# Optimization experiments

Measured on AMD Instinct MI355X. Metric: run time of the kernel, lower is better.

Reference implementation:

```python
import jax, jax.numpy as jnp
import numpy as np


def setup_inputs() -> dict:
    key = jax.random.key(0)
    ks = jax.random.split(key, 5)
    B, S, D, H, DK = 2, 2048, 1024, 16, 64
    scale = 1.0 / np.sqrt(D)
    return {
        "x": jax.random.normal(ks[0], (B, S, D), dtype=jnp.float32),
        "Wq": jax.random.normal(ks[1], (H, D, DK), dtype=jnp.float32) * scale,
        "Wk": jax.random.normal(ks[2], (H, D, DK), dtype=jnp.float32) * scale,
        "Wv": jax.random.normal(ks[3], (H, D, DK), dtype=jnp.float32) * scale,
        "Wo": jax.random.normal(ks[4], (D, D), dtype=jnp.float32) * scale,
    }


def reference(x, Wq, Wk, Wv, Wo):
    # x: (B, S, D); Wq/Wk/Wv: (H, D, d_k); Wo: (D, D) torch-Linear convention (y = c @ Wo.T)
    B, S, D = x.shape
    H, _, dk = Wq.shape
    Q = jnp.einsum('bsd,hdk->bhsk', x, Wq)  # (B,H,S,dk)
    K = jnp.einsum('bsd,hdk->bhsk', x, Wk)
    V = jnp.einsum('bsd,hdk->bhsk', x, Wv)
    scores = jnp.einsum('bhqk,bhsk->bhqs', Q, K) / jnp.sqrt(jnp.float32(dk))  # (B,H,S,S)
    causal = jnp.tril(jnp.ones((S, S), dtype=bool))
    scores = jnp.where(causal[None, None, :, :], scores, -jnp.inf)
    weights = jax.nn.softmax(scores, axis=-1)
    out = jnp.einsum('bhqs,bhsk->bhqk', weights, V)  # (B,H,S,dk)
    concat = out.transpose(0, 2, 1, 3).reshape(B, S, H * dk)  # heads concatenated h-major
    return concat @ Wo.T
```

## Files before the change

### kernel.cpp

```cpp
#include <hip/hip_runtime.h>

typedef unsigned short u16;
typedef unsigned int u32;
typedef __bf16 bf16x8 __attribute__((ext_vector_type(8)));
typedef float f32x4 __attribute__((ext_vector_type(4)));
typedef u16 u16x8 __attribute__((ext_vector_type(8)));
typedef u16 u16x4 __attribute__((ext_vector_type(4)));
typedef u32 u32x4 __attribute__((ext_vector_type(4)));

#define NH 16
#define DKK 64
#define SQ 2048
#define DD 1024

#define AS1 __attribute__((address_space(1)))
#define AS3 __attribute__((address_space(3)))

#define QSCALE 0.1803368925f
#define CBIAS 8.0f

#define WAIT4 do { asm volatile("s_waitcnt vmcnt(4)" ::: "memory"); \
                   __builtin_amdgcn_sched_barrier(0); } while (0)
#define WAIT0 do { asm volatile("s_waitcnt vmcnt(0)" ::: "memory"); \
                   __builtin_amdgcn_sched_barrier(0); } while (0)
#define BAR   __builtin_amdgcn_s_barrier()

__device__ inline u16 f2bf(float f) {
  union { float f; u32 u; } v; v.f = f;
  u32 u = v.u;
  u += 0x7FFFu + ((u >> 16) & 1u);
  return (u16)(u >> 16);
}

__device__ __forceinline__ u32 cvtpk(float lo, float hi) {
  u32 r;
  asm("v_cvt_pk_bf16_f32 %0, %1, %2" : "=v"(r) : "v"(lo), "v"(hi));
  return r;
}

__device__ inline u16x8 cvt8(const float* p) {
  float4 a = *(const float4*)p;
  float4 b = *(const float4*)(p + 4);
  u16x8 v;
  v[0] = f2bf(a.x); v[1] = f2bf(a.y); v[2] = f2bf(a.z); v[3] = f2bf(a.w);
  v[4] = f2bf(b.x); v[5] = f2bf(b.y); v[6] = f2bf(b.z); v[7] = f2bf(b.w);
  return v;
}

__device__ __forceinline__ void gload16(const u16* g, u16* l) {
  __builtin_amdgcn_global_load_lds((const AS1 u32*)(const void*)g,
                                   (AS3 u32*)(void*)l, 16, 0, 0);
}

__global__ __launch_bounds__(256) void prep_kernel(const float* __restrict__ x,
                                                   u16* __restrict__ xb,
                                                   const float* __restrict__ Wo,
                                                   u16* __restrict__ Wob,
                                                   const float* __restrict__ Wq,
                                                   const float* __restrict__ Wk,
                                                   const float* __restrict__ Wv,
                                                   u16* __restrict__ WT) {
  __shared__ u16 sm[64][72];
  int bid = blockIdx.x;
  int tid = threadIdx.x;
  if (bid < 2560) {
    const float* src; u16* dst; size_t base;
    if (bid < 2048) { src = x;  dst = xb;  base = (size_t)bid * 2048; }
    else            { src = Wo; dst = Wob; base = (size_t)(bid - 2048) * 2048; }
    size_t off = base + (size_t)tid * 8;
    *(u16x8*)&dst[off] = cvt8(&src[off]);
    return;
  }
  int wid = bid - 2560;
  int t = wid >> 8;
  int rem = wid & 255;
  int h = rem >> 4;
  int d0 = (rem & 15) * 64;
  const float* src = (t == 0) ? Wq : (t == 1) ? Wk : Wv;
  for (int j = 0; j < 2; ++j) {
    int idx = tid + j * 256;
    int r = idx >> 3;
    int c0 = (idx & 7) * 8;
    *(u16x8*)&sm[r][c0] = cvt8(&src[(h * DD + d0 + r) * DKK + c0]);
  }
  __syncthreads();
  for (int j = 0; j < 2; ++j) {
    int idx = tid + j * 256;
    int r2 = idx >> 3;
    int c0 = (idx & 7) * 8;
    u16x8 vv;
    for (int i = 0; i < 8; ++i) vv[i] = sm[c0 + i][r2];
    int n = t * 1024 + h * 64 + r2;
    *(u16x8*)&WT[n * DD + d0 + c0] = vv;
  }
}

__global__ __launch_bounds__(256) void gemm128(const u16* __restrict__ A,
                                               const u16* __restrict__ Bm,
                                               int mode,
                                               u16* __restrict__ o0,
                                               u16* __restrict__ o1,
                                               u16* __restrict__ o2,
                                               float* __restrict__ of) {
  __shared__ u16 As[2][128 * 32];
  __shared__ u16 Bs[2][128 * 32];
  const int K = 1024;
  int m0 = blockIdx.x * 128;
  int n0 = blockIdx.y * 128;
  int tid = threadIdx.x;
  int w = tid >> 6, l = tid & 63;
  int lg = l >> 4, lr = l & 15;
  int wr = w >> 1, wc = w & 1;

  int srow = w * 32 + (l >> 2);
  int sg = (l & 3) ^ ((l >> 3) & 3);
  const u16* gA = A + (size_t)(m0 + srow) * K + sg * 8;
  const u16* gB = Bm + (size_t)(n0 + srow) * K + sg * 8;
  int gsw = (lr >> 1) & 3;

  #define GSTAGE(buf, k0)                              \
    do {                                               \
      gload16(gA + (k0), &As[buf][w * 1024]);          \
      gload16(gA + (k0) + 16 * K, &As[buf][w * 1024 + 512]); \
      gload16(gB + (k0), &Bs[buf][w * 1024]);          \
      gload16(gB + (k0) + 16 * K, &Bs[buf][w * 1024 + 512]); \
    } while (0)

  f32x4 acc[4][4] = {};
  GSTAGE(0, 0);
  for (int kt = 0; kt < 32; ++kt) {
    int buf = kt & 1;
    if (kt < 31) { GSTAGE(buf ^ 1, (kt + 1) * 32); WAIT4; }
    else         { WAIT0; }
    BAR;
    bf16x8 a[4], b[4];
    #pragma unroll
    for (int m = 0; m < 4; ++m)
      a[m] = *(const bf16x8*)&As[buf][(wr * 64 + m * 16 + lr) * 32 + ((lg ^ gsw) * 8)];
    #pragma unroll
    for (int n = 0; n < 4; ++n)
      b[n] = *(const bf16x8*)&Bs[buf][(wc * 64 + n * 16 + lr) * 32 + ((lg ^ gsw) * 8)];
    #pragma unroll
    for (int m = 0; m < 4; ++m)
      #pragma unroll
      for (int n = 0; n < 4; ++n)
        acc[m][n] = __builtin_amdgcn_mfma_f32_16x16x32_bf16(a[m], b[n], acc[m][n], 0, 0, 0);
    BAR;
  }
  #undef GSTAGE

  if (mode == 1) {
    int mbase = m0 + wr * 64 + lg * 4;
    int nbase = n0 + wc * 64 + lr;
    #pragma unroll
    for (int m = 0; m < 4; ++m)
      #pragma unroll
      for (int n = 0; n < 4; ++n)
        #pragma unroll
        for (int rr = 0; rr < 4; ++rr)
          of[(size_t)(mbase + m * 16 + rr) * 1024 + nbase + n * 16] = acc[m][n][rr];
  } else {
    int t = n0 >> 10;
    int h = (((n0 & 1023) + wc * 64) >> 6);
    int bq = m0 >> 11;
    int sbase = (m0 & 2047) + wr * 64 + lg * 4;
    if (t < 2) {
      float sc = (t == 0) ? QSCALE : 1.0f;
      u16* o = (t == 0) ? o0 : o1;
      u16* op = o + (size_t)(bq * NH + h) * SQ * DKK;
      #pragma unroll
      for (int m = 0; m < 4; ++m)
        #pragma unroll
        for (int n = 0; n < 4; ++n)
          #pragma unroll
          for (int rr = 0; rr < 4; ++rr)
            op[(size_t)(sbase + m * 16 + rr) * DKK + n * 16 + lr] = f2bf(acc[m][n][rr] * sc);
    } else {
      u16* op = o2 + (size_t)(bq * NH + h) * DKK * SQ;
      int Sb = (m0 & 2047) + wr * 64;
      #pragma unroll
      for (int m = 0; m < 4; ++m)
        #pragma unroll
        for (int n = 0; n < 4; ++n) {
          u16x4 vv;
          #pragma unroll
          for (int rr = 0; rr < 4; ++rr) vv[rr] = f2bf(acc[m][n][rr]);
          *(u16x4*)&op[(size_t)(n * 16 + lr) * SQ + Sb + (m >> 1) * 32 + lg * 8 + (m & 1) * 4] = vv;
        }
    }
  }
}

__global__ __launch_bounds__(256) void attn_kernel(const u16* __restrict__ Q,
                                                   const u16* __restrict__ Kg,
                                                   const u16* __restrict__ Vt,
                                                   u16* __restrict__ Cc) {
  __shared__ u16 Ks[2][64 * 64];
  __shared__ u16 Vs[2][64 * 64];
  int bh = blockIdx.x;
  int y = blockIdx.y;
  int a = y & 7, bsel = y >> 3;
  int s = (bsel == 0) ? 2 * a : (bsel == 1) ? 2 * a + 1
        : (bsel == 2) ? 30 - 2 * a : 31 - 2 * a;
  int tid = threadIdx.x;
  int w = tid >> 6, l = tid & 63;
  int lg = l >> 4, lr = l & 15;
  const u16* Qp = Q + (size_t)bh * SQ * DKK;
  const u16* Kp = Kg + (size_t)bh * SQ * DKK;
  const u16* Vp = Vt + (size_t)bh * DKK * SQ;
  int b = bh >> 4, h = bh & 15;
  int cur = 0;

  int lrow8 = l >> 3;
  int swz = (l & 7) ^ lrow8;
  int r7 = lr & 7;
  const u16* kSrc0 = Kp + (size_t)(w * 16 + lrow8) * DKK + swz * 8;
  const u16* kSrc1 = Kp + (size_t)(w * 16 + 8 + lrow8) * DKK + swz * 8;
  const u16* vSrc0 = Vp + (size_t)(w * 16 + lrow8) * SQ + swz * 8;
  const u16* vSrc1 = Vp + (size_t)(w * 16 + 8 + lrow8) * SQ + swz * 8;

  #define STAGE(buf, j0)                                                  \
    do {                                                                  \
      gload16(kSrc0 + (size_t)(j0) * DKK, &Ks[buf][(w * 16) * 64]);       \
      gload16(kSrc1 + (size_t)(j0) * DKK, &Ks[buf][(w * 16 + 8) * 64]);   \
      gload16(vSrc0 + (j0), &Vs[buf][(w * 16) * 64]);                     \
      gload16(vSrc1 + (j0), &Vs[buf][(w * 16 + 8) * 64]);                 \
    } while (0)

  int qrow = s * 64 + w * 16 + lr;
  bf16x8 qf0 = *(const bf16x8*)&Qp[(size_t)qrow * DKK + lg * 8];
  bf16x8 qf1 = *(const bf16x8*)&Qp[(size_t)qrow * DKK + 32 + lg * 8];

  STAGE(0, 0);

  f32x4 o[4] = {};
  float lpart = 0.f;

  for (int jt = 0; jt <= s; ++jt) {
    if (jt < s) { STAGE(cur ^ 1, (jt + 1) * 64); WAIT4; }
    else        { WAIT0; }
    BAR;

    float p[16];
    __builtin_amdgcn_s_setprio(1);
    #pragma unroll
    for (int c = 0; c < 4; ++c) {
      int R = c * 16 + lr;
      const u16* kr = &Ks[cur][R * 64];
      bf16x8 k0 = *(const bf16x8*)&kr[(lg ^ r7) * 8];
      bf16x8 k1 = *(const bf16x8*)&kr[((4 + lg) ^ r7) * 8];
      f32x4 z = {};
      z = __builtin_amdgcn_mfma_f32_16x16x32_bf16(k0, qf0, z, 0, 0, 0);
      z = __builtin_amdgcn_mfma_f32_16x16x32_bf16(k1, qf1, z, 0, 0, 0);
      #pragma unroll
      for (int rr = 0; rr < 4; ++rr) p[c * 4 + rr] = z[rr];
    }
    __builtin_amdgcn_s_setprio(0);
    if (jt == s) {
      int j0 = jt * 64;
      #pragma unroll
      for (int c = 0; c < 4; ++c)
        #pragma unroll
        for (int rr = 0; rr < 4; ++rr) {
          int kv = j0 + c * 16 + lg * 4 + rr;
          if (kv > qrow) p[c * 4 + rr] = -1e30f;
        }
    }
    float su = 0.f;
    #pragma unroll
    for (int i = 0; i < 16; ++i) { p[i] = exp2f(p[i] - CBIAS); su += p[i]; }
    lpart += su;
    union { u32x4 w; bf16x8 v; } pk0, pk1;
    pk0.w[0] = cvtpk(p[0],  p[1]);
    pk0.w[1] = cvtpk(p[2],  p[3]);
    pk0.w[2] = cvtpk(p[4],  p[5]);
    pk0.w[3] = cvtpk(p[6],  p[7]);
    pk1.w[0] = cvtpk(p[8],  p[9]);
    pk1.w[1] = cvtpk(p[10], p[11]);
    pk1.w[2] = cvtpk(p[12], p[13]);
    pk1.w[3] = cvtpk(p[14], p[15]);
    {
      bf16x8 pa0 = pk0.v, pa1 = pk1.v;
      __builtin_amdgcn_s_setprio(1);
      #pragma unroll
      for (int n = 0; n < 4; ++n) {
        int R2 = n * 16 + lr;
        bf16x8 vb0 = *(const bf16x8*)&Vs[cur][R2 * 64 + ((lg ^ r7) * 8)];
        o[n] = __builtin_amdgcn_mfma_f32_16x16x32_bf16(pa0, vb0, o[n], 0, 0, 0);
        bf16x8 vb1 = *(const bf16x8*)&Vs[cur][R2 * 64 + (((4 + lg) ^ r7) * 8)];
        o[n] = __builtin_amdgcn_mfma_f32_16x16x32_bf16(pa1, vb1, o[n], 0, 0, 0);
      }
      __builtin_amdgcn_s_setprio(0);
    }
    BAR;
    cur ^= 1;
  }

  float lsum = lpart;
  lsum += __shfl_xor(lsum, 16, 64);
  lsum += __shfl_xor(lsum, 32, 64);
  float lrow[4];
  #pragma unroll
  for (int rr = 0; rr < 4; ++rr) lrow[rr] = __shfl(lsum, lg * 4 + rr, 64);
  int srow = s * 64 + w * 16 + lg * 4;
  #pragma unroll
  for (int n = 0; n < 4; ++n)
    #pragma unroll
    for (int rr = 0; rr < 4; ++rr) {
      float val = o[n][rr] / lrow[rr];
      Cc[((size_t)(b * SQ + srow + rr)) * DD + h * DKK + n * 16 + lr] = f2bf(val);
    }
  #undef STAGE
}

extern "C" void kernel_launch(void* const* d_in, const int* in_sizes, int n_in,
                              void* d_out, int out_size, void* d_ws, size_t ws_size,
                              hipStream_t stream) {
  (void)in_sizes; (void)n_in; (void)out_size; (void)ws_size;
  const float* x  = (const float*)d_in[0];
  const float* Wq = (const float*)d_in[1];
  const float* Wk = (const float*)d_in[2];
  const float* Wv = (const float*)d_in[3];
  const float* Wo = (const float*)d_in[4];
  float* out = (float*)d_out;
  u16* ws = (u16*)d_ws;
  u16* WT  = ws;
  u16* Qb  = WT + 3145728;
  u16* Kb  = Qb + 4194304;
  u16* Vb  = Kb + 4194304;
  u16* XC  = Vb + 4194304;
  u16* Wob = XC + 4194304;

  hipLaunchKernelGGL(prep_kernel, dim3(3328), dim3(256), 0, stream, x, XC, Wo, Wob, Wq, Wk, Wv, WT);
  hipLaunchKernelGGL(gemm128, dim3(32, 24), dim3(256), 0, stream, XC, WT, 0, Qb, Kb, Vb, (float*)nullptr);
  hipLaunchKernelGGL(attn_kernel, dim3(32, 32), dim3(256), 0, stream, Qb, Kb, Vb, XC);
  hipLaunchKernelGGL(gemm128, dim3(32, 8), dim3(256), 0, stream, XC, Wob, 1, nullptr, nullptr, nullptr, out);
}
```

Before: 114.4 us.

## Use 128-row attention tiles with 512 threads and a separate narrower Wo GEMM

The attention kernel now processes 128 query rows per block with 8 waves sharing each 64-key K/V tile, halving the grid and the K/V loads per query. Causal masking is applied on the last two tiles, and blocks are paired (p and 15-p) to balance load. The output projection moves to a dedicated gemm_wo kernel with 128x64 tiles, doubling its block count to 512 for better CU occupancy. The risk is that larger attention blocks wait on diagonal tiles with partial masking and need more registers per block.

```diff
diff --git a/kernel.cpp b/kernel.cpp
--- a/kernel.cpp
+++ b/kernel.cpp
@@ -20,6 +20,10 @@
 #define CBIAS 8.0f
 
 #define WAIT4 do { asm volatile("s_waitcnt vmcnt(4)" ::: "memory"); \
+                   __builtin_amdgcn_sched_barrier(0); } while (0)
+#define WAIT3 do { asm volatile("s_waitcnt vmcnt(3)" ::: "memory"); \
+                   __builtin_amdgcn_sched_barrier(0); } while (0)
+#define WAIT2 do { asm volatile("s_waitcnt vmcnt(2)" ::: "memory"); \
                    __builtin_amdgcn_sched_barrier(0); } while (0)
 #define WAIT0 do { asm volatile("s_waitcnt vmcnt(0)" ::: "memory"); \
                    __builtin_amdgcn_sched_barrier(0); } while (0)
@@ -97,11 +101,9 @@
 
 __global__ __launch_bounds__(256) void gemm128(const u16* __restrict__ A,
                                                const u16* __restrict__ Bm,
-                                               int mode,
                                                u16* __restrict__ o0,
                                                u16* __restrict__ o1,
-                                               u16* __restrict__ o2,
-                                               float* __restrict__ of) {
+                                               u16* __restrict__ o2) {
   __shared__ u16 As[2][128 * 32];
   __shared__ u16 Bs[2][128 * 32];
   const int K = 1024;
@@ -149,17 +151,7 @@
   }
   #undef GSTAGE
 
-  if (mode == 1) {
-    int mbase = m0 + wr * 64 + lg * 4;
-    int nbase = n0 + wc * 64 + lr;
-    #pragma unroll
-    for (int m = 0; m < 4; ++m)
-      #pragma unroll
-      for (int n = 0; n < 4; ++n)
-        #pragma unroll
-        for (int rr = 0; rr < 4; ++rr)
-          of[(size_t)(mbase + m * 16 + rr) * 1024 + nbase + n * 16] = acc[m][n][rr];
-  } else {
+  {
     int t = n0 >> 10;
     int h = (((n0 & 1023) + wc * 64) >> 6);
     int bq = m0 >> 11;
@@ -191,7 +183,66 @@
   }
 }
 
-__global__ __launch_bounds__(256) void attn_kernel(const u16* __restrict__ Q,
+__global__ __launch_bounds__(256) void gemm_wo(const u16* __restrict__ A,
+                                               const u16* __restrict__ Bm,
+                                               float* __restrict__ of) {
+  __shared__ u16 As[2][128 * 32];
+  __shared__ u16 Bs[2][64 * 32];
+  const int K = 1024;
+  int m0 = blockIdx.x * 128;
+  int n0 = blockIdx.y * 64;
+  int tid = threadIdx.x;
+  int w = tid >> 6, l = tid & 63;
+  int lg = l >> 4, lr = l & 15;
+  int wr = w >> 1, wc = w & 1;
+
+  int sg = (l & 3) ^ ((l >> 3) & 3);
+  const u16* gA = A + (size_t)(m0 + w * 32 + (l >> 2)) * K + sg * 8;
+  const u16* gB = Bm + (size_t)(n0 + w * 16 + (l >> 2)) * K + sg * 8;
+  int gsw = (lr >> 1) & 3;
+
+  #define WSTAGE(buf, k0)                              \
+    do {                                               \
+      gload16(gA + (k0), &As[buf][w * 1024]);          \
+      gload16(gA + (k0) + 16 * K, &As[buf][w * 1024 + 512]); \
+      gload16(gB + (k0), &Bs[buf][w * 512]);           \
+    } while (0)
+
+  f32x4 acc[4][2] = {};
+  WSTAGE(0, 0);
+  for (int kt = 0; kt < 32; ++kt) {
+    int buf = kt & 1;
+    if (kt < 31) { WSTAGE(buf ^ 1, (kt + 1) * 32); WAIT3; }
+    else         { WAIT0; }
+    BAR;
+    bf16x8 a[4], b[2];
+    #pragma unroll
+    for (int m = 0; m < 4; ++m)
+      a[m] = *(const bf16x8*)&As[buf][(wr * 64 + m * 16 + lr) * 32 + ((lg ^ gsw) * 8)];
+    #pragma unroll
+    for (int n = 0; n < 2; ++n)
+      b[n] = *(const bf16x8*)&Bs[buf][(wc * 32 + n * 16 + lr) * 32 + ((lg ^ gsw) * 8)];
+    #pragma unroll
+    for (int m = 0; m < 4; ++m)
+      #pragma unroll
+      for (int n = 0; n < 2; ++n)
+        acc[m][n] = __builtin_amdgcn_mfma_f32_16x16x32_bf16(a[m], b[n], acc[m][n], 0, 0, 0);
+    BAR;
+  }
+  #undef WSTAGE
+
+  int mbase = m0 + wr * 64 + lg * 4;
+  int nbase = n0 + wc * 32 + lr;
+  #pragma unroll
+  for (int m = 0; m < 4; ++m)
+    #pragma unroll
+    for (int n = 0; n < 2; ++n)
+      #pragma unroll
+      for (int rr = 0; rr < 4; ++rr)
+        of[(size_t)(mbase + m * 16 + rr) * 1024 + nbase + n * 16] = acc[m][n][rr];
+}
+
+__global__ __launch_bounds__(512) void attn_kernel(const u16* __restrict__ Q,
                                                    const u16* __restrict__ Kg,
                                                    const u16* __restrict__ Vt,
                                                    u16* __restrict__ Cc) {
@@ -199,9 +250,9 @@
   __shared__ u16 Vs[2][64 * 64];
   int bh = blockIdx.x;
   int y = blockIdx.y;
-  int a = y & 7, bsel = y >> 3;
-  int s = (bsel == 0) ? 2 * a : (bsel == 1) ? 2 * a + 1
-        : (bsel == 2) ? 30 - 2 * a : 31 - 2 * a;
+  int a = y & 7;
+  int p = (y < 8) ? a : (15 - a);
+  int nt = 2 * p + 2;
   int tid = threadIdx.x;
   int w = tid >> 6, l = tid & 63;
   int lg = l >> 4, lr = l & 15;
@@ -214,34 +265,32 @@
   int lrow8 = l >> 3;
   int swz = (l & 7) ^ lrow8;
   int r7 = lr & 7;
-  const u16* kSrc0 = Kp + (size_t)(w * 16 + lrow8) * DKK + swz * 8;
-  const u16* kSrc1 = Kp + (size_t)(w * 16 + 8 + lrow8) * DKK + swz * 8;
-  const u16* vSrc0 = Vp + (size_t)(w * 16 + lrow8) * SQ + swz * 8;
-  const u16* vSrc1 = Vp + (size_t)(w * 16 + 8 + lrow8) * SQ + swz * 8;
-
-  #define STAGE(buf, j0)                                                  \
-    do {                                                                  \
-      gload16(kSrc0 + (size_t)(j0) * DKK, &Ks[buf][(w * 16) * 64]);       \
-      gload16(kSrc1 + (size_t)(j0) * DKK, &Ks[buf][(w * 16 + 8) * 64]);   \
-      gload16(vSrc0 + (j0), &Vs[buf][(w * 16) * 64]);                     \
-      gload16(vSrc1 + (j0), &Vs[buf][(w * 16 + 8) * 64]);                 \
+  const u16* kS0 = Kp + (size_t)(w * 8 + lrow8) * DKK + swz * 8;
+  const u16* vS0 = Vp + (size_t)(w * 8 + lrow8) * SQ + swz * 8;
+
+  #define STAGE(buf)                                      \
+    do {                                                  \
+      gload16(kS0, &Ks[buf][(w * 8) * 64]);               \
+      gload16(vS0, &Vs[buf][(w * 8) * 64]);               \
+      kS0 += 64 * DKK;                                    \
+      vS0 += 64;                                          \
     } while (0)
 
-  int qrow = s * 64 + w * 16 + lr;
+  int qrow = p * 128 + w * 16 + lr;
   bf16x8 qf0 = *(const bf16x8*)&Qp[(size_t)qrow * DKK + lg * 8];
   bf16x8 qf1 = *(const bf16x8*)&Qp[(size_t)qrow * DKK + 32 + lg * 8];
 
-  STAGE(0, 0);
+  STAGE(0);
 
   f32x4 o[4] = {};
   float lpart = 0.f;
 
-  for (int jt = 0; jt <= s; ++jt) {
-    if (jt < s) { STAGE(cur ^ 1, (jt + 1) * 64); WAIT4; }
-    else        { WAIT0; }
-    BAR;
-
-    float p[16];
+  for (int jt = 0; jt < nt; ++jt) {
+    if (jt < nt - 1) { STAGE(cur ^ 1); WAIT2; }
+    else             { WAIT0; }
+    BAR;
+
+    float p16[16];
     __builtin_amdgcn_s_setprio(1);
     #pragma unroll
     for (int c = 0; c < 4; ++c) {
@@ -253,32 +302,32 @@
       z = __builtin_amdgcn_mfma_f32_16x16x32_bf16(k0, qf0, z, 0, 0, 0);
       z = __builtin_amdgcn_mfma_f32_16x16x32_bf16(k1, qf1, z, 0, 0, 0);
       #pragma unroll
-      for (int rr = 0; rr < 4; ++rr) p[c * 4 + rr] = z[rr];
+      for (int rr = 0; rr < 4; ++rr) p16[c * 4 + rr] = z[rr];
     }
     __builtin_amdgcn_s_setprio(0);
-    if (jt == s) {
+    if (jt >= 2 * p) {
       int j0 = jt * 64;
       #pragma unroll
       for (int c = 0; c < 4; ++c)
         #pragma unroll
         for (int rr = 0; rr < 4; ++rr) {
           int kv = j0 + c * 16 + lg * 4 + rr;
-          if (kv > qrow) p[c * 4 + rr] = -1e30f;
+          if (kv > qrow) p16[c * 4 + rr] = -1e30f;
         }
     }
     float su = 0.f;
     #pragma unroll
-    for (int i = 0; i < 16; ++i) { p[i] = exp2f(p[i] - CBIAS); su += p[i]; }
+    for (int i = 0; i < 16; ++i) { p16[i] = exp2f(p16[i] - CBIAS); su += p16[i]; }
     lpart += su;
     union { u32x4 w; bf16x8 v; } pk0, pk1;
-    pk0.w[0] = cvtpk(p[0],  p[1]);
-    pk0.w[1] = cvtpk(p[2],  p[3]);
-    pk0.w[2] = cvtpk(p[4],  p[5]);
-    pk0.w[3] = cvtpk(p[6],  p[7]);
-    pk1.w[0] = cvtpk(p[8],  p[9]);
-    pk1.w[1] = cvtpk(p[10], p[11]);
-    pk1.w[2] = cvtpk(p[12], p[13]);
-    pk1.w[3] = cvtpk(p[14], p[15]);
+    pk0.w[0] = cvtpk(p16[0],  p16[1]);
+    pk0.w[1] = cvtpk(p16[2],  p16[3]);
+    pk0.w[2] = cvtpk(p16[4],  p16[5]);
+    pk0.w[3] = cvtpk(p16[6],  p16[7]);
+    pk1.w[0] = cvtpk(p16[8],  p16[9]);
+    pk1.w[1] = cvtpk(p16[10], p16[11]);
+    pk1.w[2] = cvtpk(p16[12], p16[13]);
+    pk1.w[3] = cvtpk(p16[14], p16[15]);
     {
       bf16x8 pa0 = pk0.v, pa1 = pk1.v;
       __builtin_amdgcn_s_setprio(1);
@@ -302,7 +351,7 @@
   float lrow[4];
   #pragma unroll
   for (int rr = 0; rr < 4; ++rr) lrow[rr] = __shfl(lsum, lg * 4 + rr, 64);
-  int srow = s * 64 + w * 16 + lg * 4;
+  int srow = p * 128 + w * 16 + lg * 4;
   #pragma unroll
   for (int n = 0; n < 4; ++n)
     #pragma unroll
@@ -332,7 +381,7 @@
   u16* Wob = XC + 4194304;
 
   hipLaunchKernelGGL(prep_kernel, dim3(3328), dim3(256), 0, stream, x, XC, Wo, Wob, Wq, Wk, Wv, WT);
-  hipLaunchKernelGGL(gemm128, dim3(32, 24), dim3(256), 0, stream, XC, WT, 0, Qb, Kb, Vb, (float*)nullptr);
-  hipLaunchKernelGGL(attn_kernel, dim3(32, 32), dim3(256), 0, stream, Qb, Kb, Vb, XC);
-  hipLaunchKernelGGL(gemm128, dim3(32, 8), dim3(256), 0, stream, XC, Wob, 1, nullptr, nullptr, nullptr, out);
-}
+  hipLaunchKernelGGL(gemm128, dim3(32, 24), dim3(256), 0, stream, XC, WT, Qb, Kb, Vb);
+  hipLaunchKernelGGL(attn_kernel, dim3(32, 16), dim3(512), 0, stream, Qb, Kb, Vb, XC);
+  hipLaunchKernelGGL(gemm_wo, dim3(32, 16), dim3(256), 0, stream, XC, Wob, out);
+}
```

Result: no change. 113.0 us (-1.2%).
